# Kernel optimization log

Measured on AMD Instinct MI355X. Metric: run time of the kernel, lower is better.

The kernel has to match this reference:

```python
import jax, jax.numpy as jnp
import numpy as np

CLS_W = 1.0
REG_W = 1.0
POS_THR = 0.6
THR_LOW = 0.3
THR_HIGH = 0.6
N_POS = 16
N_NEG = 48
BATCH = 4096
NUM_ANCHOR = 5
FS = 17
SEARCH = 255


def make_anchors():
    # SiamRPN-style anchors: 5 aspect ratios, base size 64, stride 8, 17x17 grid
    ratios = np.array([0.33, 0.5, 1.0, 2.0, 3.0], dtype=np.float64)
    size, stride = 64.0, 8
    ws = np.sqrt(size * size / ratios)            # (K,)
    hs = ws * ratios                              # (K,)
    c = (np.arange(FS) - FS // 2) * stride + SEARCH // 2  # grid centers
    cx = np.broadcast_to(c[None, None, :], (NUM_ANCHOR, FS, FS))
    cy = np.broadcast_to(c[None, :, None], (NUM_ANCHOR, FS, FS))
    w = np.broadcast_to(ws[:, None, None], (NUM_ANCHOR, FS, FS))
    h = np.broadcast_to(hs[:, None, None], (NUM_ANCHOR, FS, FS))
    center = np.stack([cx, cy, w, h], 0).reshape(4, -1).T               # (A,4) cx,cy,w,h
    corner = np.stack([cx - w / 2, cy - h / 2, cx + w / 2, cy + h / 2], 0).reshape(4, -1).T
    return center.astype(np.float32), corner.astype(np.float32)


def setup_inputs() -> dict:
    key = jax.random.key(0)
    k1, k2, k3, k4 = jax.random.split(key, 4)
    pred_cls = jax.random.normal(k1, (BATCH, NUM_ANCHOR, FS, FS), dtype=jnp.float32)
    pred_reg = jax.random.normal(k2, (BATCH, 4, NUM_ANCHOR, FS, FS), dtype=jnp.float32)
    # valid GT boxes inside the search region, overlapping anchor sizes
    cxy = jax.random.uniform(k3, (BATCH, 2), minval=90.0, maxval=165.0)
    wh = jax.random.uniform(k4, (BATCH, 2), minval=35.0, maxval=110.0)
    gt_bbox = jnp.concatenate([cxy - wh / 2, cxy + wh / 2], axis=1).astype(jnp.float32)
    center, corner = make_anchors()
    return {
        "pred_cls": pred_cls,
        "pred_reg": pred_reg,
        "gt_bbox": gt_bbox,
        "anchor_center": jnp.asarray(center),
        "anchor_corner": jnp.asarray(corner),
    }


def jaccard(box_a, box_b):
    # box_a (N,4), box_b (A,4) in x1,y1,x2,y2 -> (N,A) IoU
    lt = jnp.maximum(box_a[:, None, :2], box_b[None, :, :2])
    rb = jnp.minimum(box_a[:, None, 2:], box_b[None, :, 2:])
    wh = jnp.clip(rb - lt, 0.0)
    inter = wh[..., 0] * wh[..., 1]
    area_a = (box_a[:, 2] - box_a[:, 0]) * (box_a[:, 3] - box_a[:, 1])
    area_b = (box_b[:, 2] - box_b[:, 0]) * (box_b[:, 3] - box_b[:, 1])
    return inter / (area_a[:, None] + area_b[None, :] - inter)


def _rand_rank(k, m, A):
    # rank of each index among masked entries under a random shuffle
    u = jax.random.uniform(k, (A,))
    s = jnp.where(m, u, jnp.inf)
    order = jnp.argsort(s)
    return jnp.zeros((A,), jnp.int32).at[order].set(jnp.arange(A, dtype=jnp.int32))


def _forward(pred_cls, pred_reg, gt_bbox, anchor_center, anchor_corner):
    N = pred_cls.shape[0]
    A = anchor_center.shape[0]
    iou = jaccard(gt_bbox, anchor_corner)                       # (N,A)
    matched = jnp.where(iou > THR_HIGH, 1.0, jnp.where(iou < THR_LOW, 0.0, -1.0))
    ks = jax.random.split(jax.random.key(42), 2 * N)
    kpos, kneg = ks[:N], ks[N:]

    def per_sample(cls, reg, gt, mask, kp, kn):
        clsf = cls.reshape(-1)                                  # (A,)
        regf = reg.reshape(4, -1).T                             # (A,4)
        pos = mask == 1.0
        neg = mask == 0.0
        n_pos = jnp.sum(pos).astype(jnp.int32)
        n_neg = jnp.sum(neg).astype(jnp.int32)
        rp = _rand_rank(kp, pos, A)
        rn = _rand_rank(kn, neg, A)
        k_p = jnp.minimum(n_pos, N_POS)                         # sampled positives
        k_n_cap = jnp.where(n_pos > 0, 3 * n_pos, N_NEG)        # int(n_pos*48/16) = 3*n_pos
        k_n = jnp.minimum(n_neg, k_n_cap)
        sel_p = pos & (rp < k_p)
        sel_n = neg & (rn < k_n)
        bce_p = jnp.logaddexp(0.0, -clsf)                       # BCEWithLogits, target 1
        bce_n = jnp.logaddexp(0.0, clsf)                        # BCEWithLogits, target 0
        denom = jnp.maximum(k_p + k_n, 1).astype(clsf.dtype)
        loss_cls_i = (jnp.sum(bce_p * sel_p) + jnp.sum(bce_n * sel_n)) / denom
        acc_i = (jnp.sum((clsf >= POS_THR) & pos) + jnp.sum((clsf < POS_THR) & (~pos))).astype(clsf.dtype) / A
        gcx = (gt[0] + gt[2]) * 0.5
        gcy = (gt[1] + gt[3]) * 0.5
        gw = gt[2] - gt[0]
        gh = gt[3] - gt[1]
        acx, acy, aw, ah = anchor_center[:, 0], anchor_center[:, 1], anchor_center[:, 2], anchor_center[:, 3]
        tgt = jnp.stack([(gcx - acx) / aw, (gcy - acy) / ah, jnp.log(gw / aw), jnp.log(gh / ah)], axis=1)
        np_safe = jnp.maximum(n_pos, 1).astype(clsf.dtype)
        loss_reg_i = jnp.where(n_pos > 0,
                               jnp.sum(((regf - tgt) ** 2) * pos[:, None]) / (4.0 * np_safe),
                               0.0)
        return loss_cls_i, loss_reg_i, acc_i

    lc, lr, ac = jax.vmap(per_sample)(pred_cls, pred_reg, gt_bbox, matched, kpos, kneg)
    loss_cls = jnp.mean(lc)
    loss_reg = jnp.mean(lr)
    acc_cls = jnp.mean(ac)
    loss_total = CLS_W * loss_cls + REG_W * loss_reg
    return loss_total, loss_cls, loss_reg, acc_cls


def reference(pred_cls, pred_reg, gt_bbox, anchor_center, anchor_corner):
    return _forward(pred_cls, pred_reg, gt_bbox, anchor_center, anchor_corner)
```

## Files before the change

### kernel.cpp

```cpp
#include <hip/hip_runtime.h>
#include <stdint.h>
#include <math.h>


#define A_TOT 1445
#define BLOCK 256
#define POS_MAX 256
#define CAND_MAX 192

__device__ __forceinline__ void tf2x32(uint32_t k0, uint32_t k1, uint32_t x0, uint32_t x1,
                                       uint32_t& o0, uint32_t& o1)
{
  const uint32_t k2 = k0 ^ k1 ^ 0x1BD11BDAu;
  x0 += k0; x1 += k1;
#define TFR(r) { x0 += x1; x1 = __builtin_rotateleft32(x1, (r)); x1 ^= x0; }
  TFR(13) TFR(15) TFR(26) TFR(6)
  x0 += k1; x1 += k2 + 1u;
  TFR(17) TFR(29) TFR(16) TFR(24)
  x0 += k2; x1 += k0 + 2u;
  TFR(13) TFR(15) TFR(26) TFR(6)
  x0 += k0; x1 += k1 + 3u;
  TFR(17) TFR(29) TFR(16) TFR(24)
  x0 += k1; x1 += k2 + 4u;
  TFR(13) TFR(15) TFR(26) TFR(6)
  x0 += k2; x1 += k0 + 5u;
#undef TFR
  o0 = x0; o1 = x1;
}

__device__ __forceinline__ float lae0(float x){
  return fmaxf(x, 0.0f) + __logf(1.0f + __expf(-fabsf(x)));
}

__global__ void __launch_bounds__(BLOCK) rpn_loss_kernel(
    const float* __restrict__ pred_cls, const float* __restrict__ pred_reg,
    const float* __restrict__ gt_bbox, const float* __restrict__ anchor_center,
    const float* __restrict__ anchor_corner,
    float* __restrict__ part,
    int N)
{
  __shared__ uint32_t s_rnm[A_TOT];
  __shared__ uint32_t s_hist[256];
  __shared__ uint32_t s_pidx[POS_MAX];
  __shared__ uint32_t s_pr[POS_MAX];
  __shared__ float    s_pcls[POS_MAX];
  __shared__ uint32_t s_cand[CAND_MAX];
  __shared__ uint32_t s_scal[4];
  __shared__ uint32_t s_key[4];
  __shared__ float    s_red[12];

  const int n   = blockIdx.x;
  const int tid = threadIdx.x;

  s_hist[tid] = 0u;
  if (tid < 4) s_scal[tid] = 0u;
  if (tid == 0){
    uint32_t a, b;
    tf2x32(0u, 42u, 0u, (uint32_t)n,       a, b); s_key[0] = a; s_key[1] = b;
    tf2x32(0u, 42u, 0u, (uint32_t)(N + n), a, b); s_key[2] = a; s_key[3] = b;
  }
  const float g0 = gt_bbox[4 * n + 0];
  const float g1 = gt_bbox[4 * n + 1];
  const float g2 = gt_bbox[4 * n + 2];
  const float g3 = gt_bbox[4 * n + 3];
  const float area_a = (g2 - g0) * (g3 - g1);
  __syncthreads();
  const uint32_t kp0 = s_key[0], kp1 = s_key[1];
  const uint32_t kn0 = s_key[2], kn1 = s_key[3];

  float accc = 0.0f;
  const float*  cls_base = pred_cls + (size_t)n * A_TOT;
  const float4* cornv = (const float4*)anchor_corner;
  for (int j = tid; j < A_TOT; j += BLOCK){
    float4 cr = cornv[j];
    float ltx = fmaxf(g0, cr.x), lty = fmaxf(g1, cr.y);
    float rbx = fminf(g2, cr.z), rby = fminf(g3, cr.w);
    float wx = fmaxf(rbx - ltx, 0.0f), wy = fmaxf(rby - lty, 0.0f);
    float inter = wx * wy;
    float area_b = (cr.z - cr.x) * (cr.w - cr.y);
    float iou = inter / (area_a + area_b - inter);
    bool pos = iou > 0.6f;
    bool neg = iou < 0.3f;
    float c = cls_base[j];
    uint32_t o0, o1;
    tf2x32(kn0, kn1, 0u, (uint32_t)j, o0, o1);
    uint32_t rn = (o0 ^ o1) >> 9;
    uint32_t enc = pos ? 2u : (neg ? 0u : 1u);
    s_rnm[j] = (rn << 2) | enc;
    if (neg) atomicAdd(&s_hist[rn >> 15], 1u);
    if (pos){
      uint32_t id = atomicAdd(&s_scal[0], 1u);
      if (id < POS_MAX){ s_pidx[id] = j; s_pcls[id] = c; }
    }
    accc += ((c >= 0.6f) == pos) ? 1.0f : 0.0f;
  }
  __syncthreads();

  const int n_pos = min((int)s_scal[0], POS_MAX);
  for (int t = tid; t < n_pos; t += BLOCK){
    uint32_t o0, o1;
    tf2x32(kp0, kp1, 0u, s_pidx[t], o0, o1);
    s_pr[t] = (o0 ^ o1) >> 9;
  }
  if (tid < 64){
    int b = tid * 4;
    uint32_t v0 = s_hist[b], v1 = s_hist[b+1], v2 = s_hist[b+2], v3 = s_hist[b+3];
    uint32_t p0 = v0, p1 = p0 + v1, p2 = p1 + v2, p3 = p2 + v3;
    uint32_t x = p3;
    #pragma unroll
    for (int off = 1; off < 64; off <<= 1){
      uint32_t t = __shfl_up(x, off, 64);
      x += (tid >= off) ? t : 0u;
    }
    uint32_t excl = x - p3;
    s_hist[b] = p0 + excl; s_hist[b+1] = p1 + excl;
    s_hist[b+2] = p2 + excl; s_hist[b+3] = p3 + excl;
  }
  __syncthreads();

  const int n_neg = (int)s_hist[255];
  const int k_p = min(n_pos, 16);
  const int k_n = min(n_neg, (n_pos > 0) ? 3 * n_pos : 48);

  if (k_n > 0 && (int)s_hist[tid] >= k_n && (tid == 0 || (int)s_hist[tid - 1] < k_n)){
    s_scal[2] = (uint32_t)tid;
    s_scal[3] = (tid == 0) ? 0u : s_hist[tid - 1];
  }

  float lc = 0.0f, lr = 0.0f;
  {
    const float gcx = (g0 + g2) * 0.5f, gcy = (g1 + g3) * 0.5f;
    const float gw = g2 - g0, gh = g3 - g1;
    const float4* cenv = (const float4*)anchor_center;
    const float* reg_base = pred_reg + (size_t)n * 4 * A_TOT;
    for (int t = tid; t < n_pos; t += BLOCK){
      uint32_t r = s_pr[t], j = s_pidx[t];
      int rank = 0;
      for (int l = 0; l < n_pos; l++){
        uint32_t r2 = s_pr[l], j2 = s_pidx[l];
        rank += (r2 < r || (r2 == r && j2 < j)) ? 1 : 0;
      }
      if (rank < k_p) lc += lae0(-s_pcls[t]);
      float4 ce = cenv[j];
      float t0 = (gcx - ce.x) / ce.z;
      float t1 = (gcy - ce.y) / ce.w;
      float t2 = __logf(gw / ce.z);
      float t3 = __logf(gh / ce.w);
      float d0 = reg_base[j]             - t0;
      float d1 = reg_base[A_TOT + j]     - t1;
      float d2 = reg_base[2 * A_TOT + j] - t2;
      float d3 = reg_base[3 * A_TOT + j] - t3;
      lr += d0 * d0 + d1 * d1 + d2 * d2 + d3 * d3;
    }
  }
  __syncthreads();

  const int Bb = (int)s_scal[2];
  const int m  = k_n - (int)s_scal[3];
  if (k_n > 0){
    for (int j = tid; j < A_TOT; j += BLOCK){
      uint32_t w = s_rnm[j];
      if ((w & 3u) == 0u){
        int bin = (int)(w >> 17);
        if (bin < Bb) lc += lae0(cls_base[j]);
        else if (bin == Bb){
          uint32_t id = atomicAdd(&s_scal[1], 1u);
          if (id < CAND_MAX) s_cand[id] = (((w >> 2) & 0x7FFFu) << 11) | (uint32_t)j;
        }
      }
    }
  }
  __syncthreads();
  const int L = min((int)s_scal[1], CAND_MAX);
  for (int c = tid; c < L; c += BLOCK){
    uint32_t my = s_cand[c];
    int rank = 0;
    for (int l = 0; l < L; l++) rank += (s_cand[l] < my) ? 1 : 0;
    if (rank < m) lc += lae0(cls_base[my & 0x7FFu]);
  }

  float v0 = lc, v1 = lr, v2 = accc;
  #pragma unroll
  for (int off = 32; off > 0; off >>= 1){
    v0 += __shfl_down(v0, off, 64);
    v1 += __shfl_down(v1, off, 64);
    v2 += __shfl_down(v2, off, 64);
  }
  const int wave = tid >> 6, lane = tid & 63;
  if (lane == 0){ s_red[wave] = v0; s_red[4 + wave] = v1; s_red[8 + wave] = v2; }
  __syncthreads();
  if (tid == 0){
    float slc = s_red[0] + s_red[1] + s_red[2] + s_red[3];
    float slr = s_red[4] + s_red[5] + s_red[6] + s_red[7];
    float sac = s_red[8] + s_red[9] + s_red[10] + s_red[11];
    int denom = k_p + k_n; if (denom < 1) denom = 1;
    part[n]         = slc / (float)denom;
    part[N + n]     = (n_pos > 0) ? (slr / (4.0f * (float)n_pos)) : 0.0f;
    part[2 * N + n] = sac * (1.0f / (float)A_TOT);
  }
}

__global__ void __launch_bounds__(256) reduce_kernel(const float* __restrict__ part,
                                                     float* __restrict__ out, int N)
{
  const int tid = threadIdx.x;
  float lc = 0.0f, lr = 0.0f, ac = 0.0f;
  for (int i = tid; i < N; i += 256){
    lc += part[i];
    lr += part[N + i];
    ac += part[2 * N + i];
  }
  __shared__ float s[12];
  #pragma unroll
  for (int off = 32; off > 0; off >>= 1){
    lc += __shfl_down(lc, off, 64);
    lr += __shfl_down(lr, off, 64);
    ac += __shfl_down(ac, off, 64);
  }
  const int wave = tid >> 6, lane = tid & 63;
  if (lane == 0){ s[wave] = lc; s[4 + wave] = lr; s[8 + wave] = ac; }
  __syncthreads();
  if (tid == 0){
    float LC = s[0] + s[1] + s[2] + s[3];
    float LR = s[4] + s[5] + s[6] + s[7];
    float AC = s[8] + s[9] + s[10] + s[11];
    float inv = 1.0f / (float)N;
    LC *= inv; LR *= inv; AC *= inv;
    out[0] = LC + LR;
    out[1] = LC;
    out[2] = LR;
    out[3] = AC;
  }
}

extern "C" void kernel_launch(void* const* d_in, const int* in_sizes, int n_in,
                              void* d_out, int out_size, void* d_ws, size_t ws_size,
                              hipStream_t stream)
{
  const float* pred_cls = (const float*)d_in[0];
  const float* pred_reg = (const float*)d_in[1];
  const float* gt_bbox  = (const float*)d_in[2];
  const float* a_center = (const float*)d_in[3];
  const float* a_corner = (const float*)d_in[4];
  float* part = (float*)d_ws;
  float* out  = (float*)d_out;

  const int N = in_sizes[2] / 4;

  hipLaunchKernelGGL(rpn_loss_kernel, dim3(N), dim3(BLOCK), 0, stream,
                     pred_cls, pred_reg, gt_bbox, a_center, a_corner, part, N);
  hipLaunchKernelGGL(reduce_kernel, dim3(1), dim3(256), 0, stream, part, out, N);
}
```

Before: 172.8 us.

## Map one sample per wavefront and keep per-anchor state in registers

Each sample is now processed by a single 64-lane wavefront instead of a 256-thread block. Four samples share a block, and every __syncthreads is removed in favour of wave-level shuffles and ballots. Per-anchor random numbers, class scores and negative flags stay in unrolled register arrays, so the shared-memory staging array and the second global reload of scores go away. In exchange, register pressure rises and the positive list is capped at 64 entries, down from 256. The grid also assumes N is divisible by 4.

```diff
diff --git a/kernel.cpp b/kernel.cpp
--- a/kernel.cpp
+++ b/kernel.cpp
@@ -4,9 +4,10 @@
 
 
 #define A_TOT 1445
-#define BLOCK 256
-#define POS_MAX 256
-#define CAND_MAX 192
+#define NITER 23
+#define WPB 4
+#define POS_MAX 64
+#define CAND_MAX 128
 
 __device__ __forceinline__ void tf2x32(uint32_t k0, uint32_t k1, uint32_t x0, uint32_t x1,
                                        uint32_t& o0, uint32_t& o1)
@@ -32,151 +33,157 @@
   return fmaxf(x, 0.0f) + __logf(1.0f + __expf(-fabsf(x)));
 }
 
-__global__ void __launch_bounds__(BLOCK) rpn_loss_kernel(
+__global__ void __launch_bounds__(WPB * 64, 4) rpn_loss_kernel(
     const float* __restrict__ pred_cls, const float* __restrict__ pred_reg,
     const float* __restrict__ gt_bbox, const float* __restrict__ anchor_center,
     const float* __restrict__ anchor_corner,
     float* __restrict__ part,
     int N)
 {
-  __shared__ uint32_t s_rnm[A_TOT];
-  __shared__ uint32_t s_hist[256];
-  __shared__ uint32_t s_pidx[POS_MAX];
-  __shared__ uint32_t s_pr[POS_MAX];
-  __shared__ float    s_pcls[POS_MAX];
-  __shared__ uint32_t s_cand[CAND_MAX];
-  __shared__ uint32_t s_scal[4];
-  __shared__ uint32_t s_key[4];
-  __shared__ float    s_red[12];
-
-  const int n   = blockIdx.x;
-  const int tid = threadIdx.x;
-
-  s_hist[tid] = 0u;
-  if (tid < 4) s_scal[tid] = 0u;
-  if (tid == 0){
-    uint32_t a, b;
-    tf2x32(0u, 42u, 0u, (uint32_t)n,       a, b); s_key[0] = a; s_key[1] = b;
-    tf2x32(0u, 42u, 0u, (uint32_t)(N + n), a, b); s_key[2] = a; s_key[3] = b;
-  }
+  __shared__ uint32_t s_hist[WPB][256];
+  __shared__ uint32_t s_cand[WPB][CAND_MAX];
+  __shared__ uint32_t s_pidx[WPB][POS_MAX];
+  __shared__ float    s_pcls[WPB][POS_MAX];
+  __shared__ uint32_t s_cnt[WPB][2];
+
+  const int w    = threadIdx.x >> 6;
+  const int lane = threadIdx.x & 63;
+  const int n    = blockIdx.x * WPB + w;
+
+  #pragma unroll
+  for (int b = 0; b < 4; b++) s_hist[w][lane * 4 + b] = 0u;
+  if (lane < 2) s_cnt[w][lane] = 0u;
+
   const float g0 = gt_bbox[4 * n + 0];
   const float g1 = gt_bbox[4 * n + 1];
   const float g2 = gt_bbox[4 * n + 2];
   const float g3 = gt_bbox[4 * n + 3];
   const float area_a = (g2 - g0) * (g3 - g1);
-  __syncthreads();
-  const uint32_t kp0 = s_key[0], kp1 = s_key[1];
-  const uint32_t kn0 = s_key[2], kn1 = s_key[3];
-
-  float accc = 0.0f;
+
+  uint32_t kp0, kp1, kn0, kn1;
+  tf2x32(0u, 42u, 0u, (uint32_t)n,       kp0, kp1);
+  tf2x32(0u, 42u, 0u, (uint32_t)(N + n), kn0, kn1);
+
   const float*  cls_base = pred_cls + (size_t)n * A_TOT;
   const float4* cornv = (const float4*)anchor_corner;
-  for (int j = tid; j < A_TOT; j += BLOCK){
-    float4 cr = cornv[j];
+
+  uint32_t rn[NITER];
+  float    cv[NITER];
+  uint32_t negbits = 0u;
+  float accc = 0.0f;
+
+  #pragma unroll
+  for (int t = 0; t < NITER; t++){
+    int j = lane + 64 * t;
+    bool valid = (j < A_TOT);
+    int jc = valid ? j : (A_TOT - 1);
+    float4 cr = cornv[jc];
+    float c = cls_base[jc];
+    cv[t] = c;
     float ltx = fmaxf(g0, cr.x), lty = fmaxf(g1, cr.y);
     float rbx = fminf(g2, cr.z), rby = fminf(g3, cr.w);
-    float wx = fmaxf(rbx - ltx, 0.0f), wy = fmaxf(rby - lty, 0.0f);
-    float inter = wx * wy;
+    float inter = fmaxf(rbx - ltx, 0.0f) * fmaxf(rby - lty, 0.0f);
     float area_b = (cr.z - cr.x) * (cr.w - cr.y);
     float iou = inter / (area_a + area_b - inter);
-    bool pos = iou > 0.6f;
-    bool neg = iou < 0.3f;
-    float c = cls_base[j];
+    bool pos = valid && (iou > 0.6f);
+    bool neg = valid && (iou < 0.3f);
     uint32_t o0, o1;
     tf2x32(kn0, kn1, 0u, (uint32_t)j, o0, o1);
-    uint32_t rn = (o0 ^ o1) >> 9;
-    uint32_t enc = pos ? 2u : (neg ? 0u : 1u);
-    s_rnm[j] = (rn << 2) | enc;
-    if (neg) atomicAdd(&s_hist[rn >> 15], 1u);
+    uint32_t r = (o0 ^ o1) >> 9;
+    rn[t] = r;
+    if (neg){ negbits |= (1u << t); atomicAdd(&s_hist[w][r >> 15], 1u); }
     if (pos){
-      uint32_t id = atomicAdd(&s_scal[0], 1u);
-      if (id < POS_MAX){ s_pidx[id] = j; s_pcls[id] = c; }
-    }
-    accc += ((c >= 0.6f) == pos) ? 1.0f : 0.0f;
-  }
-  __syncthreads();
-
-  const int n_pos = min((int)s_scal[0], POS_MAX);
-  for (int t = tid; t < n_pos; t += BLOCK){
-    uint32_t o0, o1;
-    tf2x32(kp0, kp1, 0u, s_pidx[t], o0, o1);
-    s_pr[t] = (o0 ^ o1) >> 9;
-  }
-  if (tid < 64){
-    int b = tid * 4;
-    uint32_t v0 = s_hist[b], v1 = s_hist[b+1], v2 = s_hist[b+2], v3 = s_hist[b+3];
-    uint32_t p0 = v0, p1 = p0 + v1, p2 = p1 + v2, p3 = p2 + v3;
-    uint32_t x = p3;
+      uint32_t id = atomicAdd(&s_cnt[w][0], 1u);
+      if (id < POS_MAX){ s_pidx[w][id] = (uint32_t)j; s_pcls[w][id] = c; }
+    }
+    if (valid) accc += ((c >= 0.6f) == pos) ? 1.0f : 0.0f;
+  }
+
+  const int n_pos = min((int)s_cnt[w][0], POS_MAX);
+  const int k_p = min(n_pos, 16);
+
+  uint32_t S0, S1, S2, S3;
+  {
+    int b = lane * 4;
+    uint32_t v0 = s_hist[w][b], v1 = s_hist[w][b+1], v2 = s_hist[w][b+2], v3 = s_hist[w][b+3];
+    S0 = v0; S1 = S0 + v1; S2 = S1 + v2; S3 = S2 + v3;
+    uint32_t x = S3;
     #pragma unroll
     for (int off = 1; off < 64; off <<= 1){
-      uint32_t t = __shfl_up(x, off, 64);
-      x += (tid >= off) ? t : 0u;
-    }
-    uint32_t excl = x - p3;
-    s_hist[b] = p0 + excl; s_hist[b+1] = p1 + excl;
-    s_hist[b+2] = p2 + excl; s_hist[b+3] = p3 + excl;
-  }
-  __syncthreads();
-
-  const int n_neg = (int)s_hist[255];
-  const int k_p = min(n_pos, 16);
+      uint32_t tmp = __shfl_up(x, off, 64);
+      if (lane >= off) x += tmp;
+    }
+    uint32_t excl = x - S3;
+    S0 += excl; S1 += excl; S2 += excl; S3 += excl;
+    s_hist[w][b] = S0; s_hist[w][b+1] = S1; s_hist[w][b+2] = S2; s_hist[w][b+3] = S3;
+  }
+  const int n_neg = (int)__shfl(S3, 63, 64);
   const int k_n = min(n_neg, (n_pos > 0) ? 3 * n_pos : 48);
 
-  if (k_n > 0 && (int)s_hist[tid] >= k_n && (tid == 0 || (int)s_hist[tid - 1] < k_n)){
-    s_scal[2] = (uint32_t)tid;
-    s_scal[3] = (tid == 0) ? 0u : s_hist[tid - 1];
+  int Bb = 256, m = 0;
+  if (k_n > 0){
+    unsigned long long bal = __ballot(S3 >= (uint32_t)k_n);
+    int fl = __ffsll((unsigned long long)bal) - 1;
+    uint32_t t0 = __shfl(S0, fl, 64), t1 = __shfl(S1, fl, 64), t2 = __shfl(S2, fl, 64);
+    int sub = (t0 >= (uint32_t)k_n) ? 0 : ((t1 >= (uint32_t)k_n) ? 1 : ((t2 >= (uint32_t)k_n) ? 2 : 3));
+    Bb = fl * 4 + sub;
+    uint32_t before = (Bb == 0) ? 0u : s_hist[w][Bb - 1];
+    m = k_n - (int)before;
   }
 
   float lc = 0.0f, lr = 0.0f;
-  {
-    const float gcx = (g0 + g2) * 0.5f, gcy = (g1 + g3) * 0.5f;
-    const float gw = g2 - g0, gh = g3 - g1;
-    const float4* cenv = (const float4*)anchor_center;
-    const float* reg_base = pred_reg + (size_t)n * 4 * A_TOT;
-    for (int t = tid; t < n_pos; t += BLOCK){
-      uint32_t r = s_pr[t], j = s_pidx[t];
-      int rank = 0;
-      for (int l = 0; l < n_pos; l++){
-        uint32_t r2 = s_pr[l], j2 = s_pidx[l];
-        rank += (r2 < r || (r2 == r && j2 < j)) ? 1 : 0;
-      }
-      if (rank < k_p) lc += lae0(-s_pcls[t]);
-      float4 ce = cenv[j];
+  if (n_pos > 0){
+    uint32_t myr = 0u, myj = 0u; float myc = 0.0f;
+    if (lane < n_pos){
+      myj = s_pidx[w][lane];
+      myc = s_pcls[w][lane];
+      uint32_t o0, o1;
+      tf2x32(kp0, kp1, 0u, myj, o0, o1);
+      myr = (o0 ^ o1) >> 9;
+    }
+    int rank = 0;
+    for (int l = 0; l < n_pos; l++){
+      uint32_t r2 = __shfl(myr, l, 64), j2 = __shfl(myj, l, 64);
+      if (lane < n_pos && (r2 < myr || (r2 == myr && j2 < myj))) rank++;
+    }
+    if (lane < n_pos){
+      if (rank < k_p) lc += lae0(-myc);
+      float gcx = (g0 + g2) * 0.5f, gcy = (g1 + g3) * 0.5f;
+      float gw = g2 - g0, gh = g3 - g1;
+      float4 ce = ((const float4*)anchor_center)[myj];
+      const float* reg_base = pred_reg + (size_t)n * 4 * A_TOT;
       float t0 = (gcx - ce.x) / ce.z;
       float t1 = (gcy - ce.y) / ce.w;
       float t2 = __logf(gw / ce.z);
       float t3 = __logf(gh / ce.w);
-      float d0 = reg_base[j]             - t0;
-      float d1 = reg_base[A_TOT + j]     - t1;
-      float d2 = reg_base[2 * A_TOT + j] - t2;
-      float d3 = reg_base[3 * A_TOT + j] - t3;
-      lr += d0 * d0 + d1 * d1 + d2 * d2 + d3 * d3;
-    }
-  }
-  __syncthreads();
-
-  const int Bb = (int)s_scal[2];
-  const int m  = k_n - (int)s_scal[3];
+      float d0 = reg_base[myj]             - t0;
+      float d1 = reg_base[A_TOT + myj]     - t1;
+      float d2 = reg_base[2 * A_TOT + myj] - t2;
+      float d3 = reg_base[3 * A_TOT + myj] - t3;
+      lr = d0 * d0 + d1 * d1 + d2 * d2 + d3 * d3;
+    }
+  }
+
   if (k_n > 0){
-    for (int j = tid; j < A_TOT; j += BLOCK){
-      uint32_t w = s_rnm[j];
-      if ((w & 3u) == 0u){
-        int bin = (int)(w >> 17);
-        if (bin < Bb) lc += lae0(cls_base[j]);
+    #pragma unroll
+    for (int t = 0; t < NITER; t++){
+      if (negbits & (1u << t)){
+        int bin = (int)(rn[t] >> 15);
+        if (bin < Bb) lc += lae0(cv[t]);
         else if (bin == Bb){
-          uint32_t id = atomicAdd(&s_scal[1], 1u);
-          if (id < CAND_MAX) s_cand[id] = (((w >> 2) & 0x7FFFu) << 11) | (uint32_t)j;
+          uint32_t id = atomicAdd(&s_cnt[w][1], 1u);
+          if (id < CAND_MAX)
+            s_cand[w][id] = ((rn[t] & 0x7FFFu) << 11) | (uint32_t)(lane + 64 * t);
         }
       }
     }
-  }
-  __syncthreads();
-  const int L = min((int)s_scal[1], CAND_MAX);
-  for (int c = tid; c < L; c += BLOCK){
-    uint32_t my = s_cand[c];
-    int rank = 0;
-    for (int l = 0; l < L; l++) rank += (s_cand[l] < my) ? 1 : 0;
-    if (rank < m) lc += lae0(cls_base[my & 0x7FFu]);
+    const int L = min((int)s_cnt[w][1], CAND_MAX);
+    for (int c = lane; c < L; c += 64){
+      uint32_t my = s_cand[w][c];
+      int rank = 0;
+      for (int l = 0; l < L; l++) rank += (s_cand[w][l] < my) ? 1 : 0;
+      if (rank < m) lc += lae0(cls_base[my & 0x7FFu]);
+    }
   }
 
   float v0 = lc, v1 = lr, v2 = accc;
@@ -186,17 +193,11 @@
     v1 += __shfl_down(v1, off, 64);
     v2 += __shfl_down(v2, off, 64);
   }
-  const int wave = tid >> 6, lane = tid & 63;
-  if (lane == 0){ s_red[wave] = v0; s_red[4 + wave] = v1; s_red[8 + wave] = v2; }
-  __syncthreads();
-  if (tid == 0){
-    float slc = s_red[0] + s_red[1] + s_red[2] + s_red[3];
-    float slr = s_red[4] + s_red[5] + s_red[6] + s_red[7];
-    float sac = s_red[8] + s_red[9] + s_red[10] + s_red[11];
+  if (lane == 0){
     int denom = k_p + k_n; if (denom < 1) denom = 1;
-    part[n]         = slc / (float)denom;
-    part[N + n]     = (n_pos > 0) ? (slr / (4.0f * (float)n_pos)) : 0.0f;
-    part[2 * N + n] = sac * (1.0f / (float)A_TOT);
+    part[n]         = v0 / (float)denom;
+    part[N + n]     = (n_pos > 0) ? (v1 / (4.0f * (float)n_pos)) : 0.0f;
+    part[2 * N + n] = v2 * (1.0f / (float)A_TOT);
   }
 }
 
@@ -247,7 +248,7 @@
 
   const int N = in_sizes[2] / 4;
 
-  hipLaunchKernelGGL(rpn_loss_kernel, dim3(N), dim3(BLOCK), 0, stream,
+  hipLaunchKernelGGL(rpn_loss_kernel, dim3(N / WPB), dim3(WPB * 64), 0, stream,
                      pred_cls, pred_reg, gt_bbox, a_center, a_corner, part, N);
   hipLaunchKernelGGL(reduce_kernel, dim3(1), dim3(256), 0, stream, part, out, N);
 }
```

New measurement: 167.2 us. 3.2% less time.
